# Kernel optimization log

Measured on AMD Instinct MI355X. Metric: run time of the kernel, lower is better.

## Reference

```python
import jax, jax.numpy as jnp
import numpy as np

N_NODES = 50000
N_EDGES = 800000
N_SCALES = 4
D_IN = 128
D_HID = 128


def gcn_conv(x, W, b, src, dst, ew, n):
    # PyG GCNConv: h = x @ W; add self loops (weight 1); symmetric normalization
    # deg computed over destination with edge weights; out = scatter(norm * h[src]) + b
    h = x @ W
    loops = jnp.arange(n)
    src_f = jnp.concatenate([src, loops])
    dst_f = jnp.concatenate([dst, loops])
    ew_f = jnp.concatenate([ew, jnp.ones((n,), x.dtype)])
    deg = jax.ops.segment_sum(ew_f, dst_f, num_segments=n)
    dinv = jnp.where(deg > 0, jax.lax.rsqrt(deg), jnp.zeros((), x.dtype))
    norm = dinv[src_f] * ew_f * dinv[dst_f]  # [E+n]
    out = jax.ops.segment_sum(h[src_f] * norm[:, None], dst_f, num_segments=n)
    return out + b


def setup_inputs() -> dict:
    key = jax.random.key(0)
    ks = jax.random.split(key, 8)
    x = jax.random.normal(ks[0], (N_NODES, D_IN), dtype=jnp.float32)
    edge_index = jax.random.randint(ks[1], (N_SCALES, 2, N_EDGES), 0, N_NODES, dtype=jnp.int64)
    edge_weight = jax.random.uniform(ks[2], (N_SCALES, N_EDGES), dtype=jnp.float32)
    s = 1.0 / np.sqrt(D_IN)
    W0 = jax.random.uniform(ks[3], (D_IN, D_HID), jnp.float32, -s, s)
    b0 = jnp.zeros((D_HID,), jnp.float32)
    W1 = jax.random.uniform(ks[4], (D_HID, D_HID), jnp.float32, -s, s)
    b1 = jnp.zeros((D_HID,), jnp.float32)
    prelu_a = 0.25 * jnp.ones((D_HID,), jnp.float32)  # torch PReLU default init
    return {"x": x, "edge_index": edge_index, "edge_weight": edge_weight,
            "W0": W0, "b0": b0, "W1": W1, "b1": b1, "prelu_a": prelu_a}


def reference(x, edge_index, edge_weight, W0, b0, W1, b1, prelu_a):
    n = x.shape[0]
    prelu = lambda z: jnp.where(z > 0, z, prelu_a * z)
    outs = []
    for t in range(edge_index.shape[0]):  # small fixed number of scales
        src, dst = edge_index[t, 0], edge_index[t, 1]
        ew = edge_weight[t]
        z = prelu(gcn_conv(x, W0, b0, src, dst, ew, n))
        z = prelu(gcn_conv(z, W1, b1, src, dst, ew, n))
        outs.append(z)
    return jnp.stack(outs)  # [nm_scale, N, hidden]
```

## Files before the change

kernel.cpp:

```cpp
#include <hip/hip_runtime.h>

#define NN 50000
#define NE 800000
#define NS 4
#define NT (NS * NN)
#define D 128
#define SB2 782
#define EW_SCALE 262144.0f
#define EW_INV (1.0f / 262144.0f)

typedef unsigned long long ull;
typedef __attribute__((ext_vector_type(8))) short bf16x8;
typedef __attribute__((ext_vector_type(4))) float f32x4;

__device__ __forceinline__ unsigned short f2bf(float f) {
  unsigned int u = __float_as_uint(f);
  u += 0x7fffu + ((u >> 16) & 1u);
  return (unsigned short)(u >> 16);
}
__device__ __forceinline__ float bf2f(unsigned short h) {
  return __uint_as_float((unsigned int)h << 16);
}


__global__ __launch_bounds__(256) void gemm_plain_bf16out(
    const float* __restrict__ X, const float* __restrict__ W,
    unsigned short* __restrict__ O, int M) {
  __shared__ float xs[64 * 130];
  __shared__ float ws[32 * 128];
  const int tid = threadIdx.x;
  const int r0 = blockIdx.x * 64;
  for (int i = tid; i < 64 * 64; i += 256) {
    int row = i >> 6, kh = i & 63;
    float2 v = make_float2(0.f, 0.f);
    int gr = r0 + row;
    if (gr < M) v = *(const float2*)&X[(size_t)gr * D + kh * 2];
    *(float2*)&xs[row * 130 + kh * 2] = v;
  }
  const int tx = tid & 15, ty = tid >> 4;
  const int c0 = tx * 4;
  const int c1 = 64 + tx * 4;
  float acc[4][8];
#pragma unroll
  for (int i = 0; i < 4; i++)
#pragma unroll
    for (int j = 0; j < 8; j++) acc[i][j] = 0.f;

  for (int kc = 0; kc < 4; kc++) {
    __syncthreads();
    for (int i = tid; i < 32 * 32; i += 256) {
      ((float4*)ws)[i] = ((const float4*)(W + kc * 32 * D))[i];
    }
    __syncthreads();
#pragma unroll 4
    for (int k2 = 0; k2 < 32; k2++) {
      const int k = kc * 32 + k2;
      float a[4];
#pragma unroll
      for (int j = 0; j < 4; j++) a[j] = xs[(ty * 4 + j) * 130 + k];
      float4 b0 = *(const float4*)&ws[k2 * 128 + c0];
      float4 b1 = *(const float4*)&ws[k2 * 128 + c1];
      float b[8] = {b0.x, b0.y, b0.z, b0.w, b1.x, b1.y, b1.z, b1.w};
#pragma unroll
      for (int i = 0; i < 4; i++)
#pragma unroll
        for (int j = 0; j < 8; j++) acc[i][j] += a[i] * b[j];
    }
  }
#pragma unroll
  for (int i = 0; i < 4; i++) {
    int gr = r0 + ty * 4 + i;
    if (gr < M) {
      ushort4 o0, o1;
      o0.x = f2bf(acc[i][0]); o0.y = f2bf(acc[i][1]);
      o0.z = f2bf(acc[i][2]); o0.w = f2bf(acc[i][3]);
      o1.x = f2bf(acc[i][4]); o1.y = f2bf(acc[i][5]);
      o1.z = f2bf(acc[i][6]); o1.w = f2bf(acc[i][7]);
      *(ushort4*)&O[(size_t)gr * D + c0] = o0;
      *(ushort4*)&O[(size_t)gr * D + c1] = o1;
    }
  }
}

__global__ __launch_bounds__(256) void prep_w1_k(const float* __restrict__ W,
                                                 unsigned short* __restrict__ Wsw) {
  int idx = blockIdx.x * 256 + threadIdx.x;
  int j = idx & 7, lane = (idx >> 3) & 63, s = (idx >> 9) & 3, bn = idx >> 11;
  float v = W[(s * 32 + ((lane >> 4) * 8) + j) * D + bn * 16 + (lane & 15)];
  unsigned short hi = f2bf(v);
  float lo = v - bf2f(hi);
  Wsw[idx] = hi;
  Wsw[16384 + idx] = f2bf(lo);
}

__global__ __launch_bounds__(256) void gemm_inplace_mfma_k(
    unsigned short* __restrict__ ZhA, const unsigned short* __restrict__ Wsw) {
  const int t = blockIdx.y;
  unsigned short* Z = ZhA + (size_t)t * NN * D;
  const int tid = threadIdx.x;
  const int wv = tid >> 6, l = tid & 63;
  const int r0 = blockIdx.x * 64 + wv * 16;
  const int mrow = r0 + (l & 15);
  const int arow = mrow < NN ? mrow : NN - 1;
  bf16x8 a[4];
#pragma unroll
  for (int s = 0; s < 4; s++)
    a[s] = *(const bf16x8*)&Z[(size_t)arow * D + s * 32 + (l >> 4) * 8];
  const int orow0 = r0 + (l >> 4) * 4;
#pragma unroll
  for (int bn = 0; bn < 8; bn++) {
    f32x4 acc = {0.f, 0.f, 0.f, 0.f};
#pragma unroll
    for (int s = 0; s < 4; s++) {
      bf16x8 blo = *(const bf16x8*)&Wsw[16384 + ((bn * 4 + s) * 64 + l) * 8];
      bf16x8 bhi = *(const bf16x8*)&Wsw[((bn * 4 + s) * 64 + l) * 8];
      acc = __builtin_amdgcn_mfma_f32_16x16x32_bf16(a[s], blo, acc, 0, 0, 0);
      acc = __builtin_amdgcn_mfma_f32_16x16x32_bf16(a[s], bhi, acc, 0, 0, 0);
    }
    const int col = bn * 16 + (l & 15);
#pragma unroll
    for (int i = 0; i < 4; i++) {
      int row = orow0 + i;
      if (row < NN) Z[(size_t)row * D + col] = f2bf(acc[i]);
    }
  }
}


__global__ __launch_bounds__(256) void initp_k(ull* __restrict__ packed, int n) {
  int i = blockIdx.x * 256 + threadIdx.x;
  if (i < n) packed[i] = 0ULL;
}

__global__ __launch_bounds__(256) void countpos_all_k(const int* __restrict__ ei,
                                                      const float* __restrict__ ewA,
                                                      ull* __restrict__ pack8,
                                                      int* __restrict__ posA) {
  const int t = blockIdx.y;
  const int e0 = blockIdx.x * 1024 + threadIdx.x;
  const size_t cOff = (size_t)(blockIdx.x & 7) * NT;
  const int* dst = ei + (size_t)t * 2 * NE + NE;
  const float* ew = ewA + (size_t)t * NE;
  int d[4];
  float w[4];
  bool va[4];
#pragma unroll
  for (int q = 0; q < 4; q++) {
    int e = e0 + q * 256;
    va[q] = e < NE;
    d[q] = 0;
    w[q] = 0.f;
    if (va[q]) {
      d[q] = dst[e];
      w[q] = ew[e];
    }
  }
  ull old[4];
#pragma unroll
  for (int q = 0; q < 4; q++) {
    if (va[q]) {
      ull add = (1ULL << 32) | (ull)__float2uint_rn(w[q] * EW_SCALE);
      old[q] = atomicAdd(&pack8[cOff + t * NN + d[q]], add);
    }
  }
#pragma unroll
  for (int q = 0; q < 4; q++) {
    if (va[q]) posA[(size_t)t * NE + e0 + q * 256] = (int)(old[q] >> 32);
  }
}

__global__ __launch_bounds__(256) void unpack_scan_k(const ull* __restrict__ pack8,
                                                     float* __restrict__ dinvA,
                                                     int* __restrict__ cntA,
                                                     unsigned short* __restrict__ cbase8,
                                                     int* __restrict__ partial) {
  __shared__ int sm[256];
  const int tid = threadIdx.x;
  const int i = blockIdx.x * 256 + tid;
  int c = 0;
  if (i < NT) {
    unsigned int wsum = 0;
    int run = 0;
#pragma unroll
    for (int k = 0; k < 8; k++) {
      ull p = pack8[(size_t)k * NT + i];
      cbase8[(size_t)k * NT + i] = (unsigned short)run;
      run += (int)(p >> 32);
      wsum += (unsigned int)(p & 0xffffffffULL);
    }
    c = run;
    cntA[i] = c;
    float deg = 1.0f + (float)wsum * EW_INV;
    dinvA[i] = rsqrtf(deg);
  }
  sm[tid] = c;
  __syncthreads();
  for (int off = 128; off > 0; off >>= 1) {
    if (tid < off) sm[tid] += sm[tid + off];
    __syncthreads();
  }
  if (tid == 0) partial[blockIdx.x] = sm[0];
}

__global__ __launch_bounds__(256) void scan_top_k(const int* __restrict__ partial,
                                                  int* __restrict__ poffs, int nb) {
  __shared__ int sm[256];
  const int t = threadIdx.x;
  const int chunk = (nb + 255) >> 8;
  const int lo = t * chunk;
  const int hi = min(lo + chunk, nb);
  int s = 0;
  for (int i = lo; i < hi; i++) s += partial[i];
  sm[t] = s;
  __syncthreads();
  for (int off = 1; off < 256; off <<= 1) {
    int u = (t >= off) ? sm[t - off] : 0;
    __syncthreads();
    sm[t] += u;
    __syncthreads();
  }
  int run = sm[t] - s;
  for (int i = lo; i < hi; i++) {
    poffs[i] = run;
    run += partial[i];
  }
}

__global__ __launch_bounds__(256) void scan_write_k(const int* __restrict__ cntA,
                                                    const int* __restrict__ poffs,
                                                    int* __restrict__ offsA) {
  __shared__ int sm[256];
  const int t = threadIdx.x;
  const int i = blockIdx.x * 256 + t;
  int v = (i < NT) ? cntA[i] : 0;
  sm[t] = v;
  __syncthreads();
  for (int off = 1; off < 256; off <<= 1) {
    int u = (t >= off) ? sm[t - off] : 0;
    __syncthreads();
    sm[t] += u;
    __syncthreads();
  }
  if (i < NT) offsA[i] = poffs[blockIdx.x] + sm[t] - v;
}

__global__ __launch_bounds__(256) void fill_all_k(const int* __restrict__ ei,
                                                  const float* __restrict__ ewA,
                                                  const float* __restrict__ dinvA,
                                                  const int* __restrict__ offsA,
                                                  const int* __restrict__ posA,
                                                  const unsigned short* __restrict__ cbase8,
                                                  int2* __restrict__ eeA) {
  const int t = blockIdx.y;
  const int e = blockIdx.x * 256 + threadIdx.x;
  if (e < NE) {
    const int* src = ei + (size_t)t * 2 * NE;
    const int* dst = src + NE;
    int s = src[e], d = dst[e];
    const int base = t * NN + d;
    const size_t cOff = (size_t)((e >> 10) & 7) * NT;
    float w = ewA[(size_t)t * NE + e] * dinvA[t * NN + s] * dinvA[base];
    int slot = offsA[base] + (int)cbase8[cOff + base] + posA[(size_t)t * NE + e];
    eeA[slot] = make_int2(s, __float_as_int(w));
  }
}

__global__ __launch_bounds__(256) void gather1_all_k(
    const unsigned short* __restrict__ H, const int* __restrict__ offsA,
    const int* __restrict__ cntA, const int2* __restrict__ eeA,
    const float* __restrict__ dinvA, const float* __restrict__ bias,
    const float* __restrict__ pa, unsigned short* __restrict__ ZhA) {
  const int t = blockIdx.y;
  int g = blockIdx.x * 256 + threadIdx.x;
  int wid = g >> 5;
  int lane = g & 31;
  if (wid >= NN) return;
  const int base = t * NN + wid;
  const int st = offsA[base];
  const int len = cntA[base];
  const int c = lane * 4;
  float ax = 0.f, ay = 0.f, az = 0.f, aw = 0.f;
  int j = 0;
  for (; j + 8 <= len; j += 8) {
    int2 p0 = eeA[st + j];
    int2 p1 = eeA[st + j + 1];
    int2 p2 = eeA[st + j + 2];
    int2 p3 = eeA[st + j + 3];
    int2 p4 = eeA[st + j + 4];
    int2 p5 = eeA[st + j + 5];
    int2 p6 = eeA[st + j + 6];
    int2 p7 = eeA[st + j + 7];
    ushort4 v0 = *(const ushort4*)&H[(size_t)p0.x * D + c];
    ushort4 v1 = *(const ushort4*)&H[(size_t)p1.x * D + c];
    ushort4 v2 = *(const ushort4*)&H[(size_t)p2.x * D + c];
    ushort4 v3 = *(const ushort4*)&H[(size_t)p3.x * D + c];
    ushort4 v4 = *(const ushort4*)&H[(size_t)p4.x * D + c];
    ushort4 v5 = *(const ushort4*)&H[(size_t)p5.x * D + c];
    ushort4 v6 = *(const ushort4*)&H[(size_t)p6.x * D + c];
    ushort4 v7 = *(const ushort4*)&H[(size_t)p7.x * D + c];
    float w0 = __int_as_float(p0.y), w1 = __int_as_float(p1.y);
    float w2 = __int_as_float(p2.y), w3 = __int_as_float(p3.y);
    float w4 = __int_as_float(p4.y), w5 = __int_as_float(p5.y);
    float w6 = __int_as_float(p6.y), w7 = __int_as_float(p7.y);
    ax += w0 * bf2f(v0.x) + w1 * bf2f(v1.x) + w2 * bf2f(v2.x) + w3 * bf2f(v3.x);
    ay += w0 * bf2f(v0.y) + w1 * bf2f(v1.y) + w2 * bf2f(v2.y) + w3 * bf2f(v3.y);
    az += w0 * bf2f(v0.z) + w1 * bf2f(v1.z) + w2 * bf2f(v2.z) + w3 * bf2f(v3.z);
    aw += w0 * bf2f(v0.w) + w1 * bf2f(v1.w) + w2 * bf2f(v2.w) + w3 * bf2f(v3.w);
    ax += w4 * bf2f(v4.x) + w5 * bf2f(v5.x) + w6 * bf2f(v6.x) + w7 * bf2f(v7.x);
    ay += w4 * bf2f(v4.y) + w5 * bf2f(v5.y) + w6 * bf2f(v6.y) + w7 * bf2f(v7.y);
    az += w4 * bf2f(v4.z) + w5 * bf2f(v5.z) + w6 * bf2f(v6.z) + w7 * bf2f(v7.z);
    aw += w4 * bf2f(v4.w) + w5 * bf2f(v5.w) + w6 * bf2f(v6.w) + w7 * bf2f(v7.w);
  }
  for (; j + 4 <= len; j += 4) {
    int2 p0 = eeA[st + j];
    int2 p1 = eeA[st + j + 1];
    int2 p2 = eeA[st + j + 2];
    int2 p3 = eeA[st + j + 3];
    ushort4 v0 = *(const ushort4*)&H[(size_t)p0.x * D + c];
    ushort4 v1 = *(const ushort4*)&H[(size_t)p1.x * D + c];
    ushort4 v2 = *(const ushort4*)&H[(size_t)p2.x * D + c];
    ushort4 v3 = *(const ushort4*)&H[(size_t)p3.x * D + c];
    float w0 = __int_as_float(p0.y), w1 = __int_as_float(p1.y);
    float w2 = __int_as_float(p2.y), w3 = __int_as_float(p3.y);
    ax += w0 * bf2f(v0.x) + w1 * bf2f(v1.x) + w2 * bf2f(v2.x) + w3 * bf2f(v3.x);
    ay += w0 * bf2f(v0.y) + w1 * bf2f(v1.y) + w2 * bf2f(v2.y) + w3 * bf2f(v3.y);
    az += w0 * bf2f(v0.z) + w1 * bf2f(v1.z) + w2 * bf2f(v2.z) + w3 * bf2f(v3.z);
    aw += w0 * bf2f(v0.w) + w1 * bf2f(v1.w) + w2 * bf2f(v2.w) + w3 * bf2f(v3.w);
  }
  for (; j < len; j++) {
    int2 p = eeA[st + j];
    float w = __int_as_float(p.y);
    ushort4 v = *(const ushort4*)&H[(size_t)p.x * D + c];
    ax += w * bf2f(v.x);
    ay += w * bf2f(v.y);
    az += w * bf2f(v.z);
    aw += w * bf2f(v.w);
  }
  float dv = dinvA[base];
  float d2 = dv * dv;
  ushort4 h = *(const ushort4*)&H[(size_t)wid * D + c];
  ax += d2 * bf2f(h.x) + bias[c];
  ay += d2 * bf2f(h.y) + bias[c + 1];
  az += d2 * bf2f(h.z) + bias[c + 2];
  aw += d2 * bf2f(h.w) + bias[c + 3];
  ax = ax > 0.f ? ax : pa[c] * ax;
  ay = ay > 0.f ? ay : pa[c + 1] * ay;
  az = az > 0.f ? az : pa[c + 2] * az;
  aw = aw > 0.f ? aw : pa[c + 3] * aw;
  ushort4 o;
  o.x = f2bf(ax); o.y = f2bf(ay); o.z = f2bf(az); o.w = f2bf(aw);
  *(ushort4*)&ZhA[(size_t)t * NN * D + (size_t)wid * D + c] = o;
}

__global__ __launch_bounds__(256) void gather2_all_k(
    const unsigned short* __restrict__ YA, const int* __restrict__ offsA,
    const int* __restrict__ cntA, const int2* __restrict__ eeA,
    const float* __restrict__ dinvA, const float* __restrict__ bias,
    const float* __restrict__ pa, float* __restrict__ out) {
  const int t = blockIdx.y;
  int g = blockIdx.x * 256 + threadIdx.x;
  int wid = g >> 5;
  int lane = g & 31;
  if (wid >= NN) return;
  const unsigned short* Y = YA + (size_t)t * NN * D;
  const int base = t * NN + wid;
  const int st = offsA[base];
  const int len = cntA[base];
  const int c = lane * 4;
  float ax = 0.f, ay = 0.f, az = 0.f, aw = 0.f;
  int j = 0;
  for (; j + 8 <= len; j += 8) {
    int2 p0 = eeA[st + j];
    int2 p1 = eeA[st + j + 1];
    int2 p2 = eeA[st + j + 2];
    int2 p3 = eeA[st + j + 3];
    int2 p4 = eeA[st + j + 4];
    int2 p5 = eeA[st + j + 5];
    int2 p6 = eeA[st + j + 6];
    int2 p7 = eeA[st + j + 7];
    ushort4 v0 = *(const ushort4*)&Y[(size_t)p0.x * D + c];
    ushort4 v1 = *(const ushort4*)&Y[(size_t)p1.x * D + c];
    ushort4 v2 = *(const ushort4*)&Y[(size_t)p2.x * D + c];
    ushort4 v3 = *(const ushort4*)&Y[(size_t)p3.x * D + c];
    ushort4 v4 = *(const ushort4*)&Y[(size_t)p4.x * D + c];
    ushort4 v5 = *(const ushort4*)&Y[(size_t)p5.x * D + c];
    ushort4 v6 = *(const ushort4*)&Y[(size_t)p6.x * D + c];
    ushort4 v7 = *(const ushort4*)&Y[(size_t)p7.x * D + c];
    float w0 = __int_as_float(p0.y), w1 = __int_as_float(p1.y);
    float w2 = __int_as_float(p2.y), w3 = __int_as_float(p3.y);
    float w4 = __int_as_float(p4.y), w5 = __int_as_float(p5.y);
    float w6 = __int_as_float(p6.y), w7 = __int_as_float(p7.y);
    ax += w0 * bf2f(v0.x) + w1 * bf2f(v1.x) + w2 * bf2f(v2.x) + w3 * bf2f(v3.x);
    ay += w0 * bf2f(v0.y) + w1 * bf2f(v1.y) + w2 * bf2f(v2.y) + w3 * bf2f(v3.y);
    az += w0 * bf2f(v0.z) + w1 * bf2f(v1.z) + w2 * bf2f(v2.z) + w3 * bf2f(v3.z);
    aw += w0 * bf2f(v0.w) + w1 * bf2f(v1.w) + w2 * bf2f(v2.w) + w3 * bf2f(v3.w);
    ax += w4 * bf2f(v4.x) + w5 * bf2f(v5.x) + w6 * bf2f(v6.x) + w7 * bf2f(v7.x);
    ay += w4 * bf2f(v4.y) + w5 * bf2f(v5.y) + w6 * bf2f(v6.y) + w7 * bf2f(v7.y);
    az += w4 * bf2f(v4.z) + w5 * bf2f(v5.z) + w6 * bf2f(v6.z) + w7 * bf2f(v7.z);
    aw += w4 * bf2f(v4.w) + w5 * bf2f(v5.w) + w6 * bf2f(v6.w) + w7 * bf2f(v7.w);
  }
  for (; j + 4 <= len; j += 4) {
    int2 p0 = eeA[st + j];
    int2 p1 = eeA[st + j + 1];
    int2 p2 = eeA[st + j + 2];
    int2 p3 = eeA[st + j + 3];
    ushort4 v0 = *(const ushort4*)&Y[(size_t)p0.x * D + c];
    ushort4 v1 = *(const ushort4*)&Y[(size_t)p1.x * D + c];
    ushort4 v2 = *(const ushort4*)&Y[(size_t)p2.x * D + c];
    ushort4 v3 = *(const ushort4*)&Y[(size_t)p3.x * D + c];
    float w0 = __int_as_float(p0.y), w1 = __int_as_float(p1.y);
    float w2 = __int_as_float(p2.y), w3 = __int_as_float(p3.y);
    ax += w0 * bf2f(v0.x) + w1 * bf2f(v1.x) + w2 * bf2f(v2.x) + w3 * bf2f(v3.x);
    ay += w0 * bf2f(v0.y) + w1 * bf2f(v1.y) + w2 * bf2f(v2.y) + w3 * bf2f(v3.y);
    az += w0 * bf2f(v0.z) + w1 * bf2f(v1.z) + w2 * bf2f(v2.z) + w3 * bf2f(v3.z);
    aw += w0 * bf2f(v0.w) + w1 * bf2f(v1.w) + w2 * bf2f(v2.w) + w3 * bf2f(v3.w);
  }
  for (; j < len; j++) {
    int2 p = eeA[st + j];
    float w = __int_as_float(p.y);
    ushort4 v = *(const ushort4*)&Y[(size_t)p.x * D + c];
    ax += w * bf2f(v.x);
    ay += w * bf2f(v.y);
    az += w * bf2f(v.z);
    aw += w * bf2f(v.w);
  }
  float dv = dinvA[base];
  float d2 = dv * dv;
  ushort4 h = *(const ushort4*)&Y[(size_t)wid * D + c];
  ax += d2 * bf2f(h.x) + bias[c];
  ay += d2 * bf2f(h.y) + bias[c + 1];
  az += d2 * bf2f(h.z) + bias[c + 2];
  aw += d2 * bf2f(h.w) + bias[c + 3];
  ax = ax > 0.f ? ax : pa[c] * ax;
  ay = ay > 0.f ? ay : pa[c + 1] * ay;
  az = az > 0.f ? az : pa[c + 2] * az;
  aw = aw > 0.f ? aw : pa[c + 3] * aw;
  float* outT = out + (size_t)t * NN * D;
  *(float4*)&outT[(size_t)wid * D + c] = make_float4(ax, ay, az, aw);
}


extern "C" void kernel_launch(void* const* d_in, const int* in_sizes, int n_in,
                              void* d_out, int out_size, void* d_ws, size_t ws_size,
                              hipStream_t stream) {
  const float* x = (const float*)d_in[0];
  const int* ei = (const int*)d_in[1];
  const float* ew = (const float*)d_in[2];
  const float* W0 = (const float*)d_in[3];
  const float* b0 = (const float*)d_in[4];
  const float* W1 = (const float*)d_in[5];
  const float* b1 = (const float*)d_in[6];
  const float* pa = (const float*)d_in[7];
  float* out = (float*)d_out;

  int2* eeA = (int2*)d_ws;
  int* posA = (int*)(eeA + (size_t)NS * NE);
  float* dinvA = (float*)(posA + (size_t)NS * NE);
  int* cntA = (int*)(dinvA + NT);
  int* offsA = cntA + NT;
  int* partial = offsA + NT;
  int* poffs = partial + 1024;
  unsigned short* H0h = (unsigned short*)(poffs + 1024);
  unsigned short* ZhA = H0h + (size_t)NN * D;
  unsigned short* Wsw = ZhA + (size_t)NS * NN * D;
  ull* pack8 = (ull*)H0h;
  unsigned short* cbase8 = ZhA;

  const int gGemm = (NN + 63) / 64;
  const int gEdge = (NE + 255) / 256;
  const int gEdge4 = (NE + 1023) / 1024;
  const int gInit8 = (8 * NT) / 256;
  const int gGather = (NN * 32 + 255) / 256;

  initp_k<<<gInit8, 256, 0, stream>>>(pack8, 8 * NT);
  countpos_all_k<<<dim3(gEdge4, NS), 256, 0, stream>>>(ei, ew, pack8, posA);
  unpack_scan_k<<<SB2, 256, 0, stream>>>(pack8, dinvA, cntA, cbase8, partial);
  scan_top_k<<<1, 256, 0, stream>>>(partial, poffs, SB2);
  scan_write_k<<<SB2, 256, 0, stream>>>(cntA, poffs, offsA);
  fill_all_k<<<dim3(gEdge, NS), 256, 0, stream>>>(ei, ew, dinvA, offsA, posA,
                                                  cbase8, eeA);

  gemm_plain_bf16out<<<gGemm, 256, 0, stream>>>(x, W0, H0h, NN);
  prep_w1_k<<<64, 256, 0, stream>>>(W1, Wsw);

  gather1_all_k<<<dim3(gGather, NS), 256, 0, stream>>>(H0h, offsA, cntA, eeA,
                                                       dinvA, b0, pa, ZhA);
  gemm_inplace_mfma_k<<<dim3(gGemm, NS), 256, 0, stream>>>(ZhA, Wsw);
  gather2_all_k<<<dim3(gGather, NS), 256, 0, stream>>>(ZhA, offsA, cntA, eeA,
                                                       dinvA, b1, pa, out);
}
```

Baseline: 728.6 us.

## Fuse degree counting, first GEMM and W1 prep into one launch; drop top scan

Degree/position counting, the X@W0 GEMM and the W1 split-bf16 swizzle now run as one horizontally fused kernel, with the block index choosing the role. This lets the independent GEMM overlap the atomic-heavy counting and removes two kernel launches. The single-block top-level scan is removed: each scan_write block now sums the partial totals of all earlier blocks itself. In exchange, each scan block redoes up to 782 reads, and pack8 moves into the ZhA region so it no longer aliases H0h, which is now written at the same time. The fused grid also launches many blocks for t>0 that return immediately.

```diff
diff --git a/kernel.cpp b/kernel.cpp
--- a/kernel.cpp
+++ b/kernel.cpp
@@ -22,75 +22,114 @@
   return __uint_as_float((unsigned int)h << 16);
 }
 
-
-__global__ __launch_bounds__(256) void gemm_plain_bf16out(
-    const float* __restrict__ X, const float* __restrict__ W,
-    unsigned short* __restrict__ O, int M) {
+__global__ __launch_bounds__(256) void fused_cpg_k(
+    const int* __restrict__ ei, const float* __restrict__ ewA,
+    ull* __restrict__ pack8, int* __restrict__ posA,
+    const float* __restrict__ X, const float* __restrict__ W0,
+    unsigned short* __restrict__ H0h,
+    const float* __restrict__ W1, unsigned short* __restrict__ Wsw) {
   __shared__ float xs[64 * 130];
   __shared__ float ws[32 * 128];
+  const int bx = blockIdx.x;
+  const int t = blockIdx.y;
   const int tid = threadIdx.x;
-  const int r0 = blockIdx.x * 64;
-  for (int i = tid; i < 64 * 64; i += 256) {
-    int row = i >> 6, kh = i & 63;
-    float2 v = make_float2(0.f, 0.f);
-    int gr = r0 + row;
-    if (gr < M) v = *(const float2*)&X[(size_t)gr * D + kh * 2];
-    *(float2*)&xs[row * 130 + kh * 2] = v;
-  }
-  const int tx = tid & 15, ty = tid >> 4;
-  const int c0 = tx * 4;
-  const int c1 = 64 + tx * 4;
-  float acc[4][8];
-#pragma unroll
-  for (int i = 0; i < 4; i++)
-#pragma unroll
-    for (int j = 0; j < 8; j++) acc[i][j] = 0.f;
-
-  for (int kc = 0; kc < 4; kc++) {
-    __syncthreads();
-    for (int i = tid; i < 32 * 32; i += 256) {
-      ((float4*)ws)[i] = ((const float4*)(W + kc * 32 * D))[i];
-    }
-    __syncthreads();
+
+  if (bx < 782) {
+    const int e0 = bx * 1024 + tid;
+    const size_t cOff = (size_t)(bx & 7) * NT;
+    const int* dst = ei + (size_t)t * 2 * NE + NE;
+    const float* ew = ewA + (size_t)t * NE;
+    int d[4];
+    float w[4];
+    bool va[4];
+#pragma unroll
+    for (int q = 0; q < 4; q++) {
+      int e = e0 + q * 256;
+      va[q] = e < NE;
+      d[q] = 0;
+      w[q] = 0.f;
+      if (va[q]) {
+        d[q] = dst[e];
+        w[q] = ew[e];
+      }
+    }
+    ull old[4];
+#pragma unroll
+    for (int q = 0; q < 4; q++) {
+      if (va[q]) {
+        ull add = (1ULL << 32) | (ull)__float2uint_rn(w[q] * EW_SCALE);
+        old[q] = atomicAdd(&pack8[cOff + t * NN + d[q]], add);
+      }
+    }
+#pragma unroll
+    for (int q = 0; q < 4; q++) {
+      if (va[q]) posA[(size_t)t * NE + e0 + q * 256] = (int)(old[q] >> 32);
+    }
+    return;
+  }
+  if (t != 0) return;
+
+  if (bx < 1564) {
+    const int r0 = (bx - 782) * 64;
+    for (int i = tid; i < 64 * 64; i += 256) {
+      int row = i >> 6, kh = i & 63;
+      float2 v = make_float2(0.f, 0.f);
+      int gr = r0 + row;
+      if (gr < NN) v = *(const float2*)&X[(size_t)gr * D + kh * 2];
+      *(float2*)&xs[row * 130 + kh * 2] = v;
+    }
+    const int tx = tid & 15, ty = tid >> 4;
+    const int c0 = tx * 4;
+    const int c1 = 64 + tx * 4;
+    float acc[4][8];
+#pragma unroll
+    for (int i = 0; i < 4; i++)
+#pragma unroll
+      for (int j = 0; j < 8; j++) acc[i][j] = 0.f;
+
+    for (int kc = 0; kc < 4; kc++) {
+      __syncthreads();
+      for (int i = tid; i < 32 * 32; i += 256) {
+        ((float4*)ws)[i] = ((const float4*)(W0 + kc * 32 * D))[i];
+      }
+      __syncthreads();
 #pragma unroll 4
-    for (int k2 = 0; k2 < 32; k2++) {
-      const int k = kc * 32 + k2;
-      float a[4];
-#pragma unroll
-      for (int j = 0; j < 4; j++) a[j] = xs[(ty * 4 + j) * 130 + k];
-      float4 b0 = *(const float4*)&ws[k2 * 128 + c0];
-      float4 b1 = *(const float4*)&ws[k2 * 128 + c1];
-      float b[8] = {b0.x, b0.y, b0.z, b0.w, b1.x, b1.y, b1.z, b1.w};
-#pragma unroll
-      for (int i = 0; i < 4; i++)
-#pragma unroll
-        for (int j = 0; j < 8; j++) acc[i][j] += a[i] * b[j];
-    }
-  }
-#pragma unroll
-  for (int i = 0; i < 4; i++) {
-    int gr = r0 + ty * 4 + i;
-    if (gr < M) {
-      ushort4 o0, o1;
-      o0.x = f2bf(acc[i][0]); o0.y = f2bf(acc[i][1]);
-      o0.z = f2bf(acc[i][2]); o0.w = f2bf(acc[i][3]);
-      o1.x = f2bf(acc[i][4]); o1.y = f2bf(acc[i][5]);
-      o1.z = f2bf(acc[i][6]); o1.w = f2bf(acc[i][7]);
-      *(ushort4*)&O[(size_t)gr * D + c0] = o0;
-      *(ushort4*)&O[(size_t)gr * D + c1] = o1;
-    }
-  }
-}
-
-__global__ __launch_bounds__(256) void prep_w1_k(const float* __restrict__ W,
-                                                 unsigned short* __restrict__ Wsw) {
-  int idx = blockIdx.x * 256 + threadIdx.x;
-  int j = idx & 7, lane = (idx >> 3) & 63, s = (idx >> 9) & 3, bn = idx >> 11;
-  float v = W[(s * 32 + ((lane >> 4) * 8) + j) * D + bn * 16 + (lane & 15)];
-  unsigned short hi = f2bf(v);
-  float lo = v - bf2f(hi);
-  Wsw[idx] = hi;
-  Wsw[16384 + idx] = f2bf(lo);
+      for (int k2 = 0; k2 < 32; k2++) {
+        const int k = kc * 32 + k2;
+        float a[4];
+#pragma unroll
+        for (int j = 0; j < 4; j++) a[j] = xs[(ty * 4 + j) * 130 + k];
+        float4 b0 = *(const float4*)&ws[k2 * 128 + c0];
+        float4 b1 = *(const float4*)&ws[k2 * 128 + c1];
+        float b[8] = {b0.x, b0.y, b0.z, b0.w, b1.x, b1.y, b1.z, b1.w};
+#pragma unroll
+        for (int i = 0; i < 4; i++)
+#pragma unroll
+          for (int j = 0; j < 8; j++) acc[i][j] += a[i] * b[j];
+      }
+    }
+#pragma unroll
+    for (int i = 0; i < 4; i++) {
+      int gr = r0 + ty * 4 + i;
+      if (gr < NN) {
+        ushort4 o0, o1;
+        o0.x = f2bf(acc[i][0]); o0.y = f2bf(acc[i][1]);
+        o0.z = f2bf(acc[i][2]); o0.w = f2bf(acc[i][3]);
+        o1.x = f2bf(acc[i][4]); o1.y = f2bf(acc[i][5]);
+        o1.z = f2bf(acc[i][6]); o1.w = f2bf(acc[i][7]);
+        *(ushort4*)&H0h[(size_t)gr * D + c0] = o0;
+        *(ushort4*)&H0h[(size_t)gr * D + c1] = o1;
+      }
+    }
+  } else {
+    int idx = (bx - 1564) * 256 + tid;
+    int j = idx & 7, lane = (idx >> 3) & 63, s = (idx >> 9) & 3, bn = idx >> 11;
+    float v = W1[(s * 32 + ((lane >> 4) * 8) + j) * D + bn * 16 + (lane & 15)];
+    unsigned short hi = f2bf(v);
+    float lo = v - bf2f(hi);
+    Wsw[idx] = hi;
+    Wsw[16384 + idx] = f2bf(lo);
+  }
 }
 
 __global__ __launch_bounds__(256) void gemm_inplace_mfma_k(
@@ -130,43 +169,6 @@
 __global__ __launch_bounds__(256) void initp_k(ull* __restrict__ packed, int n) {
   int i = blockIdx.x * 256 + threadIdx.x;
   if (i < n) packed[i] = 0ULL;
-}
-
-__global__ __launch_bounds__(256) void countpos_all_k(const int* __restrict__ ei,
-                                                      const float* __restrict__ ewA,
-                                                      ull* __restrict__ pack8,
-                                                      int* __restrict__ posA) {
-  const int t = blockIdx.y;
-  const int e0 = blockIdx.x * 1024 + threadIdx.x;
-  const size_t cOff = (size_t)(blockIdx.x & 7) * NT;
-  const int* dst = ei + (size_t)t * 2 * NE + NE;
-  const float* ew = ewA + (size_t)t * NE;
-  int d[4];
-  float w[4];
-  bool va[4];
-#pragma unroll
-  for (int q = 0; q < 4; q++) {
-    int e = e0 + q * 256;
-    va[q] = e < NE;
-    d[q] = 0;
-    w[q] = 0.f;
-    if (va[q]) {
-      d[q] = dst[e];
-      w[q] = ew[e];
-    }
-  }
-  ull old[4];
-#pragma unroll
-  for (int q = 0; q < 4; q++) {
-    if (va[q]) {
-      ull add = (1ULL << 32) | (ull)__float2uint_rn(w[q] * EW_SCALE);
-      old[q] = atomicAdd(&pack8[cOff + t * NN + d[q]], add);
-    }
-  }
-#pragma unroll
-  for (int q = 0; q < 4; q++) {
-    if (va[q]) posA[(size_t)t * NE + e0 + q * 256] = (int)(old[q] >> 32);
-  }
 }
 
 __global__ __launch_bounds__(256) void unpack_scan_k(const ull* __restrict__ pack8,
@@ -202,36 +204,23 @@
   if (tid == 0) partial[blockIdx.x] = sm[0];
 }
 
-__global__ __launch_bounds__(256) void scan_top_k(const int* __restrict__ partial,
-                                                  int* __restrict__ poffs, int nb) {
-  __shared__ int sm[256];
-  const int t = threadIdx.x;
-  const int chunk = (nb + 255) >> 8;
-  const int lo = t * chunk;
-  const int hi = min(lo + chunk, nb);
-  int s = 0;
-  for (int i = lo; i < hi; i++) s += partial[i];
-  sm[t] = s;
-  __syncthreads();
-  for (int off = 1; off < 256; off <<= 1) {
-    int u = (t >= off) ? sm[t - off] : 0;
-    __syncthreads();
-    sm[t] += u;
-    __syncthreads();
-  }
-  int run = sm[t] - s;
-  for (int i = lo; i < hi; i++) {
-    poffs[i] = run;
-    run += partial[i];
-  }
-}
-
 __global__ __launch_bounds__(256) void scan_write_k(const int* __restrict__ cntA,
-                                                    const int* __restrict__ poffs,
+                                                    const int* __restrict__ partial,
                                                     int* __restrict__ offsA) {
   __shared__ int sm[256];
   const int t = threadIdx.x;
-  const int i = blockIdx.x * 256 + t;
+  const int bx = blockIdx.x;
+  int s = 0;
+  for (int i = t; i < bx; i += 256) s += partial[i];
+  sm[t] = s;
+  __syncthreads();
+  for (int off = 128; off > 0; off >>= 1) {
+    if (t < off) sm[t] += sm[t + off];
+    __syncthreads();
+  }
+  const int base = sm[0];
+  __syncthreads();
+  const int i = bx * 256 + t;
   int v = (i < NT) ? cntA[i] : 0;
   sm[t] = v;
   __syncthreads();
@@ -241,7 +230,7 @@
     sm[t] += u;
     __syncthreads();
   }
-  if (i < NT) offsA[i] = poffs[blockIdx.x] + sm[t] - v;
+  if (i < NT) offsA[i] = base + sm[t] - v;
 }
 
 __global__ __launch_bounds__(256) void fill_all_k(const int* __restrict__ ei,
@@ -463,25 +452,23 @@
   unsigned short* H0h = (unsigned short*)(poffs + 1024);
   unsigned short* ZhA = H0h + (size_t)NN * D;
   unsigned short* Wsw = ZhA + (size_t)NS * NN * D;
-  ull* pack8 = (ull*)H0h;
   unsigned short* cbase8 = ZhA;
+  ull* pack8 = (ull*)(ZhA + (size_t)8 * NT);
 
   const int gGemm = (NN + 63) / 64;
   const int gEdge = (NE + 255) / 256;
-  const int gEdge4 = (NE + 1023) / 1024;
   const int gInit8 = (8 * NT) / 256;
   const int gGather = (NN * 32 + 255) / 256;
+  const int gFused = 782 + 782 + 64;
 
   initp_k<<<gInit8, 256, 0, stream>>>(pack8, 8 * NT);
-  countpos_all_k<<<dim3(gEdge4, NS), 256, 0, stream>>>(ei, ew, pack8, posA);
+  fused_cpg_k<<<dim3(gFused, NS), 256, 0, stream>>>(ei, ew, pack8, posA,
+                                                    x, W0, H0h, W1, Wsw);
+
   unpack_scan_k<<<SB2, 256, 0, stream>>>(pack8, dinvA, cntA, cbase8, partial);
-  scan_top_k<<<1, 256, 0, stream>>>(partial, poffs, SB2);
-  scan_write_k<<<SB2, 256, 0, stream>>>(cntA, poffs, offsA);
+  scan_write_k<<<SB2, 256, 0, stream>>>(cntA, partial, offsA);
   fill_all_k<<<dim3(gEdge, NS), 256, 0, stream>>>(ei, ew, dinvA, offsA, posA,
                                                   cbase8, eeA);
-
-  gemm_plain_bf16out<<<gGemm, 256, 0, stream>>>(x, W0, H0h, NN);
-  prep_w1_k<<<64, 256, 0, stream>>>(W1, Wsw);
 
   gather1_all_k<<<dim3(gGather, NS), 256, 0, stream>>>(H0h, offsA, cntA, eeA,
                                                        dinvA, b0, pa, ZhA);
```

Result: faster. 700.3 us (-3.9%).
